# Kernel optimization log

Hardware: AMD Instinct MI355X
Metric: run time of the kernel (lower is better)

Reference implementation:

```python
import jax, jax.numpy as jnp
import numpy as np

B, P, N, C, H, E, HORIZON = 4, 8, 10000, 64, 256, 160000, 4


def setup_inputs() -> dict:
    key = jax.random.key(0)
    ks = jax.random.split(key, 32)
    rn = lambda k, shape, s=0.05: jax.random.normal(k, shape, jnp.float32) * s
    inp = {
        "x_seq": rn(ks[0], (B, P, N, C), 1.0),
        "ei0": jax.random.randint(ks[1], (2, E), 0, N, dtype=jnp.int32),
        "ei1": jax.random.randint(ks[2], (2, E), 0, N, dtype=jnp.int32),
        "Wl0": rn(ks[3], (C, H)), "bl0": jnp.zeros((H,), jnp.float32), "Wr0": rn(ks[4], (C, H)),
        "Wl1": rn(ks[5], (C, H)), "bl1": jnp.zeros((H,), jnp.float32), "Wr1": rn(ks[6], (C, H)),
        "Wp": rn(ks[7], (C, H)), "bp": jnp.zeros((C,), jnp.float32),
    }
    i = 8
    for g in ("g1", "g2", "g3"):
        inp[g + "_Wih"] = rn(ks[i], (3 * H, H)); i += 1
        inp[g + "_Whh"] = rn(ks[i], (3 * H, H)); i += 1
        inp[g + "_bih"] = jnp.zeros((3 * H,), jnp.float32)
        inp[g + "_bhh"] = jnp.zeros((3 * H,), jnp.float32)
    return inp


def _sage(x, src, dst, Wl, bl, Wr, n_nodes):
    # PyG SAGEConv (mean aggr): lin_l(mean_j x_j) + lin_r(x_i); lin_r has no bias.
    agg = jax.ops.segment_sum(x[src], dst, num_segments=n_nodes)  # [n, C]
    cnt = jax.ops.segment_sum(jnp.ones((src.shape[0],), x.dtype), dst, num_segments=n_nodes)
    agg = agg / jnp.maximum(cnt, 1.0)[:, None]
    return agg @ Wl + bl + x @ Wr


def _gru(x, h, Wih, Whh, bih, bhh):
    gi = x @ Wih.T + bih
    gh = h @ Whh.T + bhh
    ir, iz, inn = jnp.split(gi, 3, axis=1)
    hr, hz, hn = jnp.split(gh, 3, axis=1)
    r = jax.nn.sigmoid(ir + hr)
    z = jax.nn.sigmoid(iz + hz)
    n = jnp.tanh(inn + r * hn)
    return (1.0 - z) * n + z * h


def reference(x_seq, ei0, ei1,
              Wl0, bl0, Wr0, Wl1, bl1, Wr1,
              g1_Wih, g1_Whh, g1_bih, g1_bhh,
              g2_Wih, g2_Whh, g2_bih, g2_bhh,
              g3_Wih, g3_Whh, g3_bih, g3_bhh,
              Wp, bp):
    Bn = B * N
    off = (jnp.arange(B) * N).astype(ei0.dtype)
    batch = lambda ei: (ei[:, None, :] + off[None, :, None]).reshape(2, -1)
    b0, b1 = batch(ei0), batch(ei1)

    def step(xt, h1, h2, h3):
        c = (_sage(xt, b0[0], b0[1], Wl0, bl0, Wr0, Bn)
             + _sage(xt, b1[0], b1[1], Wl1, bl1, Wr1, Bn))  # HeteroConv aggr='sum'
        c = jax.nn.relu(c)  # dropout is identity in eval
        h1 = _gru(c, h1, g1_Wih, g1_Whh, g1_bih, g1_bhh)
        h2 = _gru(h1, h2, g2_Wih, g2_Whh, g2_bih, g2_bhh)
        h3 = _gru(h2, h3, g3_Wih, g3_Whh, g3_bih, g3_bhh)
        return h1, h2, h3

    h0 = jnp.zeros((Bn, H), x_seq.dtype)
    xs = jnp.transpose(x_seq, (1, 0, 2, 3)).reshape(P, Bn, C)

    def enc_body(carry, xt):
        return step(xt, *carry), None

    (h1, h2, h3), _ = jax.lax.scan(enc_body, (h0, h0, h0), xs)

    def dec_body(carry, _):
        h1, h2, h3, xd = carry
        h1, h2, h3 = step(xd, h1, h2, h3)
        y = h3 @ Wp.T + bp  # [Bn, C]
        return (h1, h2, h3, y), y

    x_dec = x_seq[:, -1].reshape(Bn, C)
    _, ys = jax.lax.scan(dec_body, (h1, h2, h3, x_dec), None, length=HORIZON)
    # ys: [HORIZON, Bn, C] -> [B, HORIZON, N, C]
    return jnp.transpose(ys.reshape(HORIZON, B, N, C), (1, 0, 2, 3))
```

## Files before the change

kernel.cpp:

```cpp
#include <hip/hip_runtime.h>
#include <hip/hip_bf16.h>
#include <cstdint>

#define B_   4
#define P_   8
#define N_   10000
#define C_   64
#define H_   256
#define E_   160000
#define HOR_ 4
#define BN_  (B_ * N_)
#define MPAD 40064

typedef __bf16 bf16;
typedef __attribute__((ext_vector_type(8))) __bf16 bf16x8;
typedef __attribute__((ext_vector_type(4))) float f32x4;

__device__ __forceinline__ void gl2lds16(const bf16* g, bf16* l) {
    __builtin_amdgcn_global_load_lds(
        (const __attribute__((address_space(1))) void*)g,
        (__attribute__((address_space(3))) void*)l, 16, 0, 0);
}

template <int BIAS, int RELU, int OUTBF, int PROJ>
__global__ __launch_bounds__(256) void gemm_k(
    const bf16* __restrict__ A, const bf16* __restrict__ Bt,
    void* __restrict__ Cp, const float* __restrict__ bias,
    int K, int Nn, int tstep)
{
    __shared__ __align__(16) bf16 As[128 * 32];
    __shared__ __align__(16) bf16 Bs[128 * 32];

    const int tid  = threadIdx.x;
    const int m0   = blockIdx.y * 128;
    const int n0   = blockIdx.x * 128;
    const int wave = tid >> 6;
    const int lane = tid & 63;
    const int wm   = (wave >> 1) << 6;
    const int wn   = (wave & 1) << 6;
    const int lr   = lane & 15;
    const int kg   = lane >> 4;

    f32x4 acc[4][4] = {};

    const int r0 = tid >> 2;
    const int k0 = (tid & 3) << 3;

    for (int kk = 0; kk < K; kk += 32) {
        const bf16* ga = A  + (size_t)(m0 + r0) * K + kk + k0;
        const bf16* gb = Bt + (size_t)(n0 + r0) * K + kk + k0;
        gl2lds16(ga,                  As + tid * 8);
        gl2lds16(ga + 64 * (size_t)K, As + 2048 + tid * 8);
        gl2lds16(gb,                  Bs + tid * 8);
        gl2lds16(gb + 64 * (size_t)K, Bs + 2048 + tid * 8);
        __syncthreads();

        bf16x8 af[4], bfv[4];
#pragma unroll
        for (int i = 0; i < 4; ++i)
            af[i] = *reinterpret_cast<const bf16x8*>(&As[(wm + i * 16 + lr) * 32 + kg * 8]);
#pragma unroll
        for (int j = 0; j < 4; ++j)
            bfv[j] = *reinterpret_cast<const bf16x8*>(&Bs[(wn + j * 16 + lr) * 32 + kg * 8]);
#pragma unroll
        for (int i = 0; i < 4; ++i)
#pragma unroll
            for (int j = 0; j < 4; ++j)
                acc[i][j] = __builtin_amdgcn_mfma_f32_16x16x32_bf16(af[i], bfv[j], acc[i][j], 0, 0, 0);
        __syncthreads();
    }

#pragma unroll
    for (int i = 0; i < 4; ++i) {
#pragma unroll
        for (int j = 0; j < 4; ++j) {
#pragma unroll
            for (int v = 0; v < 4; ++v) {
                int row = m0 + wm + i * 16 + kg * 4 + v;
                int col = n0 + wn + j * 16 + lr;
                float val = acc[i][j][v];
                if (BIAS) val += bias[col];
                if (RELU) val = fmaxf(val, 0.f);
                if (PROJ) {
                    if (col < C_ && row < BN_) {
                        int b = row / N_, n = row - b * N_;
                        reinterpret_cast<float*>(Cp)[(((size_t)b * HOR_ + tstep) * N_ + n) * C_ + col] = val;
                    }
                } else if (OUTBF) {
                    reinterpret_cast<bf16*>(Cp)[(size_t)row * Nn + col] = (bf16)val;
                } else {
                    reinterpret_cast<float*>(Cp)[(size_t)row * Nn + col] = val;
                }
            }
        }
    }
}

__global__ __launch_bounds__(256, 2) void gru_fused_k(
    const bf16* __restrict__ X, const bf16* __restrict__ Hc,
    bf16* __restrict__ Hn,
    const bf16* __restrict__ Wpk,
    const float* __restrict__ bih, const float* __restrict__ bhh)
{
    const int id    = blockIdx.x;
    const int sblk  = id >> 6;
    const int jblk  = (id >> 3) & 7;
    const int slow  = id & 7;
    const int strip = (sblk << 3) | slow;
    if (strip >= 313) return;

    __shared__ __align__(16) bf16 Xs[128 * 32];
    __shared__ __align__(16) bf16 Hs[128 * 32];

    const int tid  = threadIdx.x;
    const int m0   = strip * 128;
    const int j0   = jblk * 32;
    const int wave = tid >> 6;
    const int lane = tid & 63;
    const int wm   = (wave >> 1) << 6;
    const int wn   = (wave & 1) << 4;
    const int wv   = wave & 1;
    const int lr   = lane & 15;
    const int kg   = lane >> 4;

    f32x4 acc[4][4] = {};

    const int r0 = tid >> 2;
    const int k0 = (tid & 3) << 3;

    const bf16* wb = Wpk + (size_t)(jblk * 2 + wv) * 24576 + lane * 8;

    for (int it = 0; it < 8; ++it) {
        const int kk = it * 32;
        gl2lds16(X  + (size_t)(m0 + r0) * 256 + kk + k0,      Xs + tid * 8);
        gl2lds16(X  + (size_t)(m0 + r0 + 64) * 256 + kk + k0, Xs + 2048 + tid * 8);
        gl2lds16(Hc + (size_t)(m0 + r0) * 256 + kk + k0,      Hs + tid * 8);
        gl2lds16(Hc + (size_t)(m0 + r0 + 64) * 256 + kk + k0, Hs + 2048 + tid * 8);
        const bf16* wit = wb + it * 3072;
        bf16x8 w0 = *reinterpret_cast<const bf16x8*>(&wit[0]);
        bf16x8 w1 = *reinterpret_cast<const bf16x8*>(&wit[512]);
        bf16x8 w2 = *reinterpret_cast<const bf16x8*>(&wit[1024]);
        bf16x8 w3 = *reinterpret_cast<const bf16x8*>(&wit[1536]);
        bf16x8 w4 = *reinterpret_cast<const bf16x8*>(&wit[2048]);
        bf16x8 w5 = *reinterpret_cast<const bf16x8*>(&wit[2560]);
        __syncthreads();

        {
            bf16x8 fa[4];
#pragma unroll
            for (int i = 0; i < 4; ++i)
                fa[i] = *reinterpret_cast<const bf16x8*>(&Xs[(wm + i * 16 + lr) * 32 + kg * 8]);
#pragma unroll
            for (int i = 0; i < 4; ++i)
                acc[0][i] = __builtin_amdgcn_mfma_f32_16x16x32_bf16(fa[i], w0, acc[0][i], 0, 0, 0);
#pragma unroll
            for (int i = 0; i < 4; ++i)
                acc[1][i] = __builtin_amdgcn_mfma_f32_16x16x32_bf16(fa[i], w1, acc[1][i], 0, 0, 0);
#pragma unroll
            for (int i = 0; i < 4; ++i)
                acc[2][i] = __builtin_amdgcn_mfma_f32_16x16x32_bf16(fa[i], w2, acc[2][i], 0, 0, 0);
        }
        {
            bf16x8 fh[4];
#pragma unroll
            for (int i = 0; i < 4; ++i)
                fh[i] = *reinterpret_cast<const bf16x8*>(&Hs[(wm + i * 16 + lr) * 32 + kg * 8]);
#pragma unroll
            for (int i = 0; i < 4; ++i)
                acc[0][i] = __builtin_amdgcn_mfma_f32_16x16x32_bf16(fh[i], w3, acc[0][i], 0, 0, 0);
#pragma unroll
            for (int i = 0; i < 4; ++i)
                acc[1][i] = __builtin_amdgcn_mfma_f32_16x16x32_bf16(fh[i], w4, acc[1][i], 0, 0, 0);
#pragma unroll
            for (int i = 0; i < 4; ++i)
                acc[3][i] = __builtin_amdgcn_mfma_f32_16x16x32_bf16(fh[i], w5, acc[3][i], 0, 0, 0);
        }
        __syncthreads();
    }

    const int col = j0 + wn + lr;
    const float b_r  = bih[col]       + bhh[col];
    const float b_z  = bih[256 + col] + bhh[256 + col];
    const float bi_n = bih[512 + col];
    const float bh_n = bhh[512 + col];
#pragma unroll
    for (int i = 0; i < 4; ++i) {
#pragma unroll
        for (int v = 0; v < 4; ++v) {
            int row = m0 + wm + i * 16 + kg * 4 + v;
            float r = __fdividef(1.f, 1.f + __expf(-(acc[0][i][v] + b_r)));
            float z = __fdividef(1.f, 1.f + __expf(-(acc[1][i][v] + b_z)));
            float a = (acc[2][i][v] + bi_n) + r * (acc[3][i][v] + bh_n);
            a = fminf(fmaxf(a, -15.f), 15.f);
            float t2 = __expf(2.f * a);
            float nn = __fdividef(t2 - 1.f, t2 + 1.f);
            float hold = (float)Hc[(size_t)row * 256 + col];
            Hn[(size_t)row * 256 + col] = (bf16)((1.f - z) * nn + z * hold);
        }
    }
}

struct __attribute__((aligned(8))) bf4 { bf16 b[4]; };

__global__ __launch_bounds__(256) void gather_conv_k(
    const float* __restrict__ xbase, long long sB, long long sN,
    const int* __restrict__ rp0, const int* __restrict__ col0,
    const int* __restrict__ rp1, const int* __restrict__ col1,
    bf16* __restrict__ Aconv)
{
    int wid  = (blockIdx.x * 256 + threadIdx.x) >> 6;
    int lane = threadIdx.x & 63;
    if (wid >= BN_) return;
    int b = wid / N_;
    int n = wid - b * N_;
    int eg = lane >> 4;
    int cl = lane & 15;
    const float* xb = xbase + (size_t)b * sB;

    float4 xv = *reinterpret_cast<const float4*>(&xb[(size_t)n * sN + cl * 4]);

    float4 s0 = {0.f, 0.f, 0.f, 0.f};
    int st = rp0[n], en = rp0[n + 1];
    float d0 = fmaxf((float)(en - st), 1.f);
    for (int e = st + eg; e < en; e += 4) {
        const float4 v = *reinterpret_cast<const float4*>(&xb[(size_t)col0[e] * sN + cl * 4]);
        s0.x += v.x; s0.y += v.y; s0.z += v.z; s0.w += v.w;
    }

    float4 s1 = {0.f, 0.f, 0.f, 0.f};
    st = rp1[n]; en = rp1[n + 1];
    float d1 = fmaxf((float)(en - st), 1.f);
    for (int e = st + eg; e < en; e += 4) {
        const float4 v = *reinterpret_cast<const float4*>(&xb[(size_t)col1[e] * sN + cl * 4]);
        s1.x += v.x; s1.y += v.y; s1.z += v.z; s1.w += v.w;
    }

#pragma unroll
    for (int m = 16; m <= 32; m <<= 1) {
        s0.x += __shfl_xor(s0.x, m, 64); s0.y += __shfl_xor(s0.y, m, 64);
        s0.z += __shfl_xor(s0.z, m, 64); s0.w += __shfl_xor(s0.w, m, 64);
        s1.x += __shfl_xor(s1.x, m, 64); s1.y += __shfl_xor(s1.y, m, 64);
        s1.z += __shfl_xor(s1.z, m, 64); s1.w += __shfl_xor(s1.w, m, 64);
    }

    if (eg == 0) {
        float r0 = 1.f / d0, r1 = 1.f / d1;
        bf16* row = Aconv + (size_t)wid * 192;
        bf4 o;
        o.b[0] = (bf16)(s0.x * r0); o.b[1] = (bf16)(s0.y * r0);
        o.b[2] = (bf16)(s0.z * r0); o.b[3] = (bf16)(s0.w * r0);
        *reinterpret_cast<bf4*>(&row[cl * 4]) = o;
        o.b[0] = (bf16)xv.x; o.b[1] = (bf16)xv.y; o.b[2] = (bf16)xv.z; o.b[3] = (bf16)xv.w;
        *reinterpret_cast<bf4*>(&row[64 + cl * 4]) = o;
        o.b[0] = (bf16)(s1.x * r1); o.b[1] = (bf16)(s1.y * r1);
        o.b[2] = (bf16)(s1.z * r1); o.b[3] = (bf16)(s1.w * r1);
        *reinterpret_cast<bf4*>(&row[128 + cl * 4]) = o;
    }
}

__global__ void count_k(const int* __restrict__ ei, int* __restrict__ cnt) {
    int e = blockIdx.x * 256 + threadIdx.x;
    if (e < E_) atomicAdd(&cnt[ei[E_ + e]], 1);
}

__global__ __launch_bounds__(1024) void scan_k(
    const int* __restrict__ cnt, int* __restrict__ rp, int* __restrict__ fill)
{
    __shared__ int sums[1024];
    int t = threadIdx.x;
    const int chunk = 10;
    int lo = t * chunk;
    int hi = lo + chunk; if (hi > N_) hi = N_;
    int s = 0;
    for (int i = lo; i < hi; ++i) s += cnt[i];
    sums[t] = s;
    __syncthreads();
    for (int off = 1; off < 1024; off <<= 1) {
        int u = (t >= off) ? sums[t - off] : 0;
        __syncthreads();
        sums[t] += u;
        __syncthreads();
    }
    int base = (t == 0) ? 0 : sums[t - 1];
    for (int i = lo; i < hi; ++i) { rp[i] = base; fill[i] = base; base += cnt[i]; }
    if (t == 1023) rp[N_] = sums[1023];
}

__global__ void fill_k(const int* __restrict__ ei, int* __restrict__ fill,
                       int* __restrict__ colarr) {
    int e = blockIdx.x * 256 + threadIdx.x;
    if (e < E_) {
        int p = atomicAdd(&fill[ei[E_ + e]], 1);
        colarr[p] = ei[e];
    }
}

__global__ void pack_w_k(const float* __restrict__ Wih, const float* __restrict__ Whh,
                         bf16* __restrict__ out) {
    int idx = blockIdx.x * 256 + threadIdx.x;
    if (idx >= 6 * 256 * 256) return;
    int e    = idx & 7;
    int lane = (idx >> 3) & 63;
    int rest = idx >> 9;
    int g    = rest % 6;
    int it   = (rest / 6) & 7;
    int wj   = rest / 48;
    int row  = (wj >> 1) * 32 + (wj & 1) * 16 + (lane & 15);
    int k    = it * 32 + (lane >> 4) * 8 + e;
    float v  = (g < 3) ? Wih[(g * 256 + row) * 256 + k]
                       : Whh[((g - 3) * 256 + row) * 256 + k];
    out[idx] = (bf16)v;
}

__global__ void build_conv_bt_k(const float* __restrict__ Wl0, const float* __restrict__ Wr0,
                                const float* __restrict__ Wl1, const float* __restrict__ Wr1,
                                bf16* __restrict__ Bt) {
    int idx = blockIdx.x * 256 + threadIdx.x;
    if (idx >= 256 * 192) return;
    int n = idx / 192, k = idx - n * 192;
    float v;
    if (k < 64)       v = Wl0[k * 256 + n];
    else if (k < 128) v = Wr0[(k - 64) * 256 + n] + Wr1[(k - 64) * 256 + n];
    else              v = Wl1[(k - 128) * 256 + n];
    Bt[idx] = (bf16)v;
}

__global__ void build_conv_bias_k(const float* __restrict__ bl0, const float* __restrict__ bl1,
                                  float* __restrict__ bias) {
    int i = threadIdx.x;
    if (i < 256) bias[i] = bl0[i] + bl1[i];
}

__global__ void build_proj_k(const float* __restrict__ Wp, const float* __restrict__ bp,
                             bf16* __restrict__ Bt, float* __restrict__ bias) {
    int idx = blockIdx.x * 256 + threadIdx.x;
    if (idx < 128 * 256) {
        int n = idx >> 8, k = idx & 255;
        Bt[idx] = (bf16)(n < 64 ? Wp[n * 256 + k] : 0.f);
    }
    if (idx < 128) bias[idx] = (idx < 64) ? bp[idx] : 0.f;
}

extern "C" void kernel_launch(void* const* d_in, const int* in_sizes, int n_in,
                              void* d_out, int out_size, void* d_ws, size_t ws_size,
                              hipStream_t stream)
{
    const float* x_seq = (const float*)d_in[0];
    const int*   ei0   = (const int*)d_in[1];
    const int*   ei1   = (const int*)d_in[2];
    const float* Wl0   = (const float*)d_in[3];
    const float* bl0   = (const float*)d_in[4];
    const float* Wr0   = (const float*)d_in[5];
    const float* Wl1   = (const float*)d_in[6];
    const float* bl1   = (const float*)d_in[7];
    const float* Wr1   = (const float*)d_in[8];
    const float* Wp    = (const float*)d_in[9];
    const float* bp    = (const float*)d_in[10];
    const float* gWih[3], *gWhh[3], *gbih[3], *gbhh[3];
    for (int g = 0; g < 3; ++g) {
        gWih[g] = (const float*)d_in[11 + 4 * g];
        gWhh[g] = (const float*)d_in[12 + 4 * g];
        gbih[g] = (const float*)d_in[13 + 4 * g];
        gbhh[g] = (const float*)d_in[14 + 4 * g];
    }

    char* p = (char*)d_ws;
    auto alloc = [&](size_t bytes) -> char* {
        char* r = p; p += (bytes + 255) & ~(size_t)255; return r;
    };
    bf16*  Aconv  = (bf16*)alloc((size_t)MPAD * 192 * 2);
    bf16*  cbuf   = (bf16*)alloc((size_t)MPAD * 256 * 2);
    bf16*  hbuf[6];
    for (int g = 0; g < 6; ++g) hbuf[g] = (bf16*)alloc((size_t)MPAD * 256 * 2);
    bf16*  wpk[3];
    for (int g = 0; g < 3; ++g)
        wpk[g] = (bf16*)alloc((size_t)6 * 256 * 256 * 2);
    bf16*  btconv = (bf16*)alloc((size_t)256 * 192 * 2);
    float* bconv  = (float*)alloc(256 * 4);
    bf16*  btproj = (bf16*)alloc((size_t)128 * 256 * 2);
    float* bproj  = (float*)alloc(128 * 4);
    int* cnt0  = (int*)alloc(N_ * 4);
    int* cnt1  = (int*)alloc(N_ * 4);
    int* rp0   = (int*)alloc((N_ + 1) * 4);
    int* rp1   = (int*)alloc((N_ + 1) * 4);
    int* fill0 = (int*)alloc((N_ + 1) * 4);
    int* fill1 = (int*)alloc((N_ + 1) * 4);
    int* col0  = (int*)alloc(E_ * 4);
    int* col1  = (int*)alloc(E_ * 4);

    hipMemsetAsync(Aconv, 0, (size_t)MPAD * 192 * 2, stream);
    for (int g = 0; g < 3; ++g)
        hipMemsetAsync(hbuf[g], 0, (size_t)MPAD * 256 * 2, stream);
    hipMemsetAsync(cnt0, 0, N_ * 4, stream);
    hipMemsetAsync(cnt1, 0, N_ * 4, stream);

    for (int g = 0; g < 3; ++g)
        pack_w_k<<<1536, 256, 0, stream>>>(gWih[g], gWhh[g], wpk[g]);
    build_conv_bt_k<<<192, 256, 0, stream>>>(Wl0, Wr0, Wl1, Wr1, btconv);
    build_conv_bias_k<<<1, 256, 0, stream>>>(bl0, bl1, bconv);
    build_proj_k<<<128, 256, 0, stream>>>(Wp, bp, btproj, bproj);

    count_k<<<(E_ + 255) / 256, 256, 0, stream>>>(ei0, cnt0);
    count_k<<<(E_ + 255) / 256, 256, 0, stream>>>(ei1, cnt1);
    scan_k<<<1, 1024, 0, stream>>>(cnt0, rp0, fill0);
    scan_k<<<1, 1024, 0, stream>>>(cnt1, rp1, fill1);
    fill_k<<<(E_ + 255) / 256, 256, 0, stream>>>(ei0, fill0, col0);
    fill_k<<<(E_ + 255) / 256, 256, 0, stream>>>(ei1, fill1, col1);

    bf16 *hc[3] = { hbuf[0], hbuf[1], hbuf[2] };
    bf16 *hn[3] = { hbuf[3], hbuf[4], hbuf[5] };

    auto do_conv = [&](const float* xb, long long sB, long long sN) {
        gather_conv_k<<<10000, 256, 0, stream>>>(xb, sB, sN, rp0, col0, rp1, col1, Aconv);
        gemm_k<1, 1, 1, 0><<<dim3(2, 313, 1), 256, 0, stream>>>(
            Aconv, btconv, cbuf, bconv, 192, 256, 0);
    };
    auto do_grus = [&]() {
        gru_fused_k<<<2560, 256, 0, stream>>>(
            cbuf, hc[0], hn[0], wpk[0], gbih[0], gbhh[0]);
        gru_fused_k<<<2560, 256, 0, stream>>>(
            hn[0], hc[1], hn[1], wpk[1], gbih[1], gbhh[1]);
        gru_fused_k<<<2560, 256, 0, stream>>>(
            hn[1], hc[2], hn[2], wpk[2], gbih[2], gbhh[2]);
        for (int g = 0; g < 3; ++g) { bf16* t = hc[g]; hc[g] = hn[g]; hn[g] = t; }
    };

    for (int ps = 0; ps < P_; ++ps) {
        do_conv(x_seq + (size_t)ps * N_ * C_, (long long)P_ * N_ * C_, C_);
        do_grus();
    }

    float* out = (float*)d_out;
    for (int t = 0; t < HOR_; ++t) {
        if (t > 0)
            do_conv(out + (size_t)(t - 1) * N_ * C_, (long long)HOR_ * N_ * C_, C_);
        do_grus();
        gemm_k<1, 0, 0, 1><<<dim3(1, 313, 1), 256, 0, stream>>>(
            hc[2], btproj, out, bproj, 256, 128, t);
    }
}
```

Measured before the change: 2.583 ms.

## Retile fused GRU kernel to 32-row strips with 64 columns per block

The fused GRU GEMM block tile changes from 128 rows x 32 hidden columns to 32 rows x 64 columns. Each of the four waves now owns 16 columns across all 32 rows, and LDS staging shrinks so one load per thread fills the X and H tiles. The grid roughly doubles and occupancy is raised to 4 blocks per SM, which should improve latency hiding. In exchange, reuse of the per-wave weight fragments across rows drops, so weight traffic per output rises.

```diff
diff --git a/kernel.cpp b/kernel.cpp
--- a/kernel.cpp
+++ b/kernel.cpp
@@ -96,47 +96,42 @@
     }
 }
 
-__global__ __launch_bounds__(256, 2) void gru_fused_k(
+__global__ __launch_bounds__(256, 4) void gru_fused_k(
     const bf16* __restrict__ X, const bf16* __restrict__ Hc,
     bf16* __restrict__ Hn,
     const bf16* __restrict__ Wpk,
     const float* __restrict__ bih, const float* __restrict__ bhh)
 {
     const int id    = blockIdx.x;
-    const int sblk  = id >> 6;
-    const int jblk  = (id >> 3) & 7;
-    const int slow  = id & 7;
-    const int strip = (sblk << 3) | slow;
-    if (strip >= 313) return;
-
-    __shared__ __align__(16) bf16 Xs[128 * 32];
-    __shared__ __align__(16) bf16 Hs[128 * 32];
+    const int shi   = id >> 5;
+    const int cb    = (id >> 3) & 3;
+    const int slo   = id & 7;
+    const int strip = (shi << 3) | slo;
+    if (strip >= 1252) return;
+
+    __shared__ __align__(16) bf16 Xs[32 * 32];
+    __shared__ __align__(16) bf16 Hs[32 * 32];
 
     const int tid  = threadIdx.x;
-    const int m0   = strip * 128;
-    const int j0   = jblk * 32;
+    const int m0   = strip * 32;
     const int wave = tid >> 6;
     const int lane = tid & 63;
-    const int wm   = (wave >> 1) << 6;
-    const int wn   = (wave & 1) << 4;
-    const int wv   = wave & 1;
     const int lr   = lane & 15;
     const int kg   = lane >> 4;
 
-    f32x4 acc[4][4] = {};
-
-    const int r0 = tid >> 2;
-    const int k0 = (tid & 3) << 3;
-
-    const bf16* wb = Wpk + (size_t)(jblk * 2 + wv) * 24576 + lane * 8;
+    f32x4 acc[4][2] = {};
+
+    const int sr = (tid & 127) >> 2;
+    const int sk = (tid & 3) << 3;
+    const bf16* gsrc = (tid < 128) ? X : Hc;
+    bf16* ldst = ((tid < 128) ? Xs : Hs) + (tid & 127) * 8;
+    const bf16* grow = gsrc + (size_t)(m0 + sr) * 256 + sk;
+
+    const bf16* wb = Wpk + (size_t)(cb * 4 + wave) * 24576 + lane * 8;
 
     for (int it = 0; it < 8; ++it) {
-        const int kk = it * 32;
-        gl2lds16(X  + (size_t)(m0 + r0) * 256 + kk + k0,      Xs + tid * 8);
-        gl2lds16(X  + (size_t)(m0 + r0 + 64) * 256 + kk + k0, Xs + 2048 + tid * 8);
-        gl2lds16(Hc + (size_t)(m0 + r0) * 256 + kk + k0,      Hs + tid * 8);
-        gl2lds16(Hc + (size_t)(m0 + r0 + 64) * 256 + kk + k0, Hs + 2048 + tid * 8);
-        const bf16* wit = wb + it * 3072;
+        gl2lds16(grow + it * 32, ldst);
+        const bf16* wit = wb + (size_t)it * 3072;
         bf16x8 w0 = *reinterpret_cast<const bf16x8*>(&wit[0]);
         bf16x8 w1 = *reinterpret_cast<const bf16x8*>(&wit[512]);
         bf16x8 w2 = *reinterpret_cast<const bf16x8*>(&wit[1024]);
@@ -145,49 +140,43 @@
         bf16x8 w5 = *reinterpret_cast<const bf16x8*>(&wit[2560]);
         __syncthreads();
 
-        {
-            bf16x8 fa[4];
-#pragma unroll
-            for (int i = 0; i < 4; ++i)
-                fa[i] = *reinterpret_cast<const bf16x8*>(&Xs[(wm + i * 16 + lr) * 32 + kg * 8]);
-#pragma unroll
-            for (int i = 0; i < 4; ++i)
-                acc[0][i] = __builtin_amdgcn_mfma_f32_16x16x32_bf16(fa[i], w0, acc[0][i], 0, 0, 0);
-#pragma unroll
-            for (int i = 0; i < 4; ++i)
-                acc[1][i] = __builtin_amdgcn_mfma_f32_16x16x32_bf16(fa[i], w1, acc[1][i], 0, 0, 0);
-#pragma unroll
-            for (int i = 0; i < 4; ++i)
-                acc[2][i] = __builtin_amdgcn_mfma_f32_16x16x32_bf16(fa[i], w2, acc[2][i], 0, 0, 0);
+        bf16x8 fa[2], fh[2];
+#pragma unroll
+        for (int i = 0; i < 2; ++i) {
+            fa[i] = *reinterpret_cast<const bf16x8*>(&Xs[(i * 16 + lr) * 32 + kg * 8]);
+            fh[i] = *reinterpret_cast<const bf16x8*>(&Hs[(i * 16 + lr) * 32 + kg * 8]);
         }
-        {
-            bf16x8 fh[4];
-#pragma unroll
-            for (int i = 0; i < 4; ++i)
-                fh[i] = *reinterpret_cast<const bf16x8*>(&Hs[(wm + i * 16 + lr) * 32 + kg * 8]);
-#pragma unroll
-            for (int i = 0; i < 4; ++i)
-                acc[0][i] = __builtin_amdgcn_mfma_f32_16x16x32_bf16(fh[i], w3, acc[0][i], 0, 0, 0);
-#pragma unroll
-            for (int i = 0; i < 4; ++i)
-                acc[1][i] = __builtin_amdgcn_mfma_f32_16x16x32_bf16(fh[i], w4, acc[1][i], 0, 0, 0);
-#pragma unroll
-            for (int i = 0; i < 4; ++i)
-                acc[3][i] = __builtin_amdgcn_mfma_f32_16x16x32_bf16(fh[i], w5, acc[3][i], 0, 0, 0);
-        }
-        __syncthreads();
-    }
-
-    const int col = j0 + wn + lr;
+#pragma unroll
+        for (int i = 0; i < 2; ++i)
+            acc[0][i] = __builtin_amdgcn_mfma_f32_16x16x32_bf16(fa[i], w0, acc[0][i], 0, 0, 0);
+#pragma unroll
+        for (int i = 0; i < 2; ++i)
+            acc[1][i] = __builtin_amdgcn_mfma_f32_16x16x32_bf16(fa[i], w1, acc[1][i], 0, 0, 0);
+#pragma unroll
+        for (int i = 0; i < 2; ++i)
+            acc[2][i] = __builtin_amdgcn_mfma_f32_16x16x32_bf16(fa[i], w2, acc[2][i], 0, 0, 0);
+#pragma unroll
+        for (int i = 0; i < 2; ++i)
+            acc[0][i] = __builtin_amdgcn_mfma_f32_16x16x32_bf16(fh[i], w3, acc[0][i], 0, 0, 0);
+#pragma unroll
+        for (int i = 0; i < 2; ++i)
+            acc[1][i] = __builtin_amdgcn_mfma_f32_16x16x32_bf16(fh[i], w4, acc[1][i], 0, 0, 0);
+#pragma unroll
+        for (int i = 0; i < 2; ++i)
+            acc[3][i] = __builtin_amdgcn_mfma_f32_16x16x32_bf16(fh[i], w5, acc[3][i], 0, 0, 0);
+        __syncthreads();
+    }
+
+    const int col = cb * 64 + wave * 16 + lr;
     const float b_r  = bih[col]       + bhh[col];
     const float b_z  = bih[256 + col] + bhh[256 + col];
     const float bi_n = bih[512 + col];
     const float bh_n = bhh[512 + col];
 #pragma unroll
-    for (int i = 0; i < 4; ++i) {
+    for (int i = 0; i < 2; ++i) {
 #pragma unroll
         for (int v = 0; v < 4; ++v) {
-            int row = m0 + wm + i * 16 + kg * 4 + v;
+            int row = m0 + i * 16 + kg * 4 + v;
             float r = __fdividef(1.f, 1.f + __expf(-(acc[0][i][v] + b_r)));
             float z = __fdividef(1.f, 1.f + __expf(-(acc[1][i][v] + b_z)));
             float a = (acc[2][i][v] + bi_n) + r * (acc[3][i][v] + bh_n);
@@ -303,10 +292,10 @@
     int lane = (idx >> 3) & 63;
     int rest = idx >> 9;
     int g    = rest % 6;
-    int it   = (rest / 6) & 7;
+    int kc   = (rest / 6) & 7;
     int wj   = rest / 48;
     int row  = (wj >> 1) * 32 + (wj & 1) * 16 + (lane & 15);
-    int k    = it * 32 + (lane >> 4) * 8 + e;
+    int k    = kc * 32 + (lane >> 4) * 8 + e;
     float v  = (g < 3) ? Wih[(g * 256 + row) * 256 + k]
                        : Whh[((g - 3) * 256 + row) * 256 + k];
     out[idx] = (bf16)v;
@@ -416,11 +405,11 @@
             Aconv, btconv, cbuf, bconv, 192, 256, 0);
     };
     auto do_grus = [&]() {
-        gru_fused_k<<<2560, 256, 0, stream>>>(
+        gru_fused_k<<<5024, 256, 0, stream>>>(
             cbuf, hc[0], hn[0], wpk[0], gbih[0], gbhh[0]);
-        gru_fused_k<<<2560, 256, 0, stream>>>(
+        gru_fused_k<<<5024, 256, 0, stream>>>(
             hn[0], hc[1], hn[1], wpk[1], gbih[1], gbhh[1]);
-        gru_fused_k<<<2560, 256, 0, stream>>>(
+        gru_fused_k<<<5024, 256, 0, stream>>>(
             hn[1], hc[2], hn[2], wpk[2], gbih[2], gbhh[2]);
         for (int g = 0; g < 3; ++g) { bf16* t = hc[g]; hc[g] = hn[g]; hn[g] = t; }
     };
```

New measurement: 2.753 ms. 6.6% more time.

## Batch encoder graph convolutions for all timesteps into single gather and GEMM launches

Applied to the files above, without the earlier changes.

The encoder's SAGE convolution inputs do not depend on the recurrent state, so the gather and conv GEMM for all P timesteps are now issued as one batched launch each (grid z/y over timesteps), with per-step Aconv/cbuf slices. This removes 14 small kernel launches and gives each launch more parallel work, so the GPU is filled better. It needs roughly 8x the Aconv/cbuf workspace and falls back to the per-step path when the workspace is too small.

```diff
diff --git a/kernel.cpp b/kernel.cpp
--- a/kernel.cpp
+++ b/kernel.cpp
@@ -26,7 +26,7 @@
 __global__ __launch_bounds__(256) void gemm_k(
     const bf16* __restrict__ A, const bf16* __restrict__ Bt,
     void* __restrict__ Cp, const float* __restrict__ bias,
-    int K, int Nn, int tstep)
+    int K, int Nn, int tstep, size_t aZ, size_t cZ)
 {
     __shared__ __align__(16) bf16 As[128 * 32];
     __shared__ __align__(16) bf16 Bs[128 * 32];
@@ -41,13 +41,16 @@
     const int lr   = lane & 15;
     const int kg   = lane >> 4;
 
+    const bf16* Az = A + (size_t)blockIdx.z * aZ;
+    const size_t cBase = (size_t)blockIdx.z * cZ;
+
     f32x4 acc[4][4] = {};
 
     const int r0 = tid >> 2;
     const int k0 = (tid & 3) << 3;
 
     for (int kk = 0; kk < K; kk += 32) {
-        const bf16* ga = A  + (size_t)(m0 + r0) * K + kk + k0;
+        const bf16* ga = Az + (size_t)(m0 + r0) * K + kk + k0;
         const bf16* gb = Bt + (size_t)(n0 + r0) * K + kk + k0;
         gl2lds16(ga,                  As + tid * 8);
         gl2lds16(ga + 64 * (size_t)K, As + 2048 + tid * 8);
@@ -87,9 +90,9 @@
                         reinterpret_cast<float*>(Cp)[(((size_t)b * HOR_ + tstep) * N_ + n) * C_ + col] = val;
                     }
                 } else if (OUTBF) {
-                    reinterpret_cast<bf16*>(Cp)[(size_t)row * Nn + col] = (bf16)val;
+                    reinterpret_cast<bf16*>(Cp)[cBase + (size_t)row * Nn + col] = (bf16)val;
                 } else {
-                    reinterpret_cast<float*>(Cp)[(size_t)row * Nn + col] = val;
+                    reinterpret_cast<float*>(Cp)[cBase + (size_t)row * Nn + col] = val;
                 }
             }
         }
@@ -203,7 +206,7 @@
 struct __attribute__((aligned(8))) bf4 { bf16 b[4]; };
 
 __global__ __launch_bounds__(256) void gather_conv_k(
-    const float* __restrict__ xbase, long long sB, long long sN,
+    const float* __restrict__ xbase, long long sB, long long sN, long long sStep,
     const int* __restrict__ rp0, const int* __restrict__ col0,
     const int* __restrict__ rp1, const int* __restrict__ col1,
     bf16* __restrict__ Aconv)
@@ -215,7 +218,8 @@
     int n = wid - b * N_;
     int eg = lane >> 4;
     int cl = lane & 15;
-    const float* xb = xbase + (size_t)b * sB;
+    const float* xb = xbase + (size_t)blockIdx.y * sStep + (size_t)b * sB;
+    bf16* Ac = Aconv + (size_t)blockIdx.y * MPAD * 192;
 
     float4 xv = *reinterpret_cast<const float4*>(&xb[(size_t)n * sN + cl * 4]);
 
@@ -245,7 +249,7 @@
 
     if (eg == 0) {
         float r0 = 1.f / d0, r1 = 1.f / d1;
-        bf16* row = Aconv + (size_t)wid * 192;
+        bf16* row = Ac + (size_t)wid * 192;
         bf4 o;
         o.b[0] = (bf16)(s0.x * r0); o.b[1] = (bf16)(s0.y * r0);
         o.b[2] = (bf16)(s0.z * r0); o.b[3] = (bf16)(s0.w * r0);
@@ -364,12 +368,15 @@
         gbhh[g] = (const float*)d_in[14 + 4 * g];
     }
 
+    const int big = ws_size >= (size_t)440 * 1024 * 1024;
+    const int aSteps = big ? P_ : 1;
+
     char* p = (char*)d_ws;
     auto alloc = [&](size_t bytes) -> char* {
         char* r = p; p += (bytes + 255) & ~(size_t)255; return r;
     };
-    bf16*  Aconv  = (bf16*)alloc((size_t)MPAD * 192 * 2);
-    bf16*  cbuf   = (bf16*)alloc((size_t)MPAD * 256 * 2);
+    bf16*  Aconv  = (bf16*)alloc((size_t)aSteps * MPAD * 192 * 2);
+    bf16*  cbuf   = (bf16*)alloc((size_t)aSteps * MPAD * 256 * 2);
     bf16*  hbuf[6];
     for (int g = 0; g < 6; ++g) hbuf[g] = (bf16*)alloc((size_t)MPAD * 256 * 2);
     bf16*  wpk[3];
@@ -388,7 +395,7 @@
     int* col0  = (int*)alloc(E_ * 4);
     int* col1  = (int*)alloc(E_ * 4);
 
-    hipMemsetAsync(Aconv, 0, (size_t)MPAD * 192 * 2, stream);
+    hipMemsetAsync(Aconv, 0, (size_t)aSteps * MPAD * 192 * 2, stream);
     for (int g = 0; g < 3; ++g)
         hipMemsetAsync(hbuf[g], 0, (size_t)MPAD * 256 * 2, stream);
     hipMemsetAsync(cnt0, 0, N_ * 4, stream);
@@ -411,13 +418,14 @@
     bf16 *hn[3] = { hbuf[3], hbuf[4], hbuf[5] };
 
     auto do_conv = [&](const float* xb, long long sB, long long sN) {
-        gather_conv_k<<<10000, 256, 0, stream>>>(xb, sB, sN, rp0, col0, rp1, col1, Aconv);
+        gather_conv_k<<<dim3(10000, 1), 256, 0, stream>>>(
+            xb, sB, sN, 0, rp0, col0, rp1, col1, Aconv);
         gemm_k<1, 1, 1, 0><<<dim3(2, 313, 1), 256, 0, stream>>>(
-            Aconv, btconv, cbuf, bconv, 192, 256, 0);
+            Aconv, btconv, cbuf, bconv, 192, 256, 0, 0, 0);
     };
-    auto do_grus = [&]() {
+    auto do_grus = [&](const bf16* xin) {
         gru_fused_k<<<2560, 256, 0, stream>>>(
-            cbuf, hc[0], hn[0], wpk[0], gbih[0], gbhh[0]);
+            xin, hc[0], hn[0], wpk[0], gbih[0], gbhh[0]);
         gru_fused_k<<<2560, 256, 0, stream>>>(
             hn[0], hc[1], hn[1], wpk[1], gbih[1], gbhh[1]);
         gru_fused_k<<<2560, 256, 0, stream>>>(
@@ -425,17 +433,31 @@
         for (int g = 0; g < 3; ++g) { bf16* t = hc[g]; hc[g] = hn[g]; hn[g] = t; }
     };
 
-    for (int ps = 0; ps < P_; ++ps) {
-        do_conv(x_seq + (size_t)ps * N_ * C_, (long long)P_ * N_ * C_, C_);
-        do_grus();
-    }
-
+    if (big) {
+        gather_conv_k<<<dim3(10000, P_), 256, 0, stream>>>(
+            x_seq, (long long)P_ * N_ * C_, C_, (long long)N_ * C_,
+            rp0, col0, rp1, col1, Aconv);
+        gemm_k<1, 1, 1, 0><<<dim3(2, 313, P_), 256, 0, stream>>>(
+            Aconv, btconv, cbuf, bconv, 192, 256, 0,
+            (size_t)MPAD * 192, (size_t)MPAD * 256);
+        for (int ps = 0; ps < P_; ++ps)
+            do_grus(cbuf + (size_t)ps * MPAD * 256);
+    } else {
+        for (int ps = 0; ps < P_; ++ps) {
+            do_conv(x_seq + (size_t)ps * N_ * C_, (long long)P_ * N_ * C_, C_);
+            do_grus(cbuf);
+        }
+    }
+
+    const bf16* lastConv = big ? cbuf + (size_t)(P_ - 1) * MPAD * 256 : cbuf;
     float* out = (float*)d_out;
     for (int t = 0; t < HOR_; ++t) {
-        if (t > 0)
+        if (t > 0) {
             do_conv(out + (size_t)(t - 1) * N_ * C_, (long long)HOR_ * N_ * C_, C_);
-        do_grus();
+            lastConv = cbuf;
+        }
+        do_grus(lastConv);
         gemm_k<1, 0, 0, 1><<<dim3(1, 313, 1), 256, 0, stream>>>(
-            hc[2], btproj, out, bproj, 256, 128, t);
-    }
-}
+            hc[2], btproj, out, bproj, 256, 128, t, 0, 0);
+    }
+}
```

Result: slower. 2.651 ms (+2.6%).
